# Optimization experiments

Hardware: AMD Instinct MI355X
Metric: run time of the kernel (lower is better)

## Reference

```python
import jax, jax.numpy as jnp
import numpy as np

EPS = 1e-5

def _ln(x, g, b):
    mu = jnp.mean(x, axis=-1, keepdims=True)
    var = jnp.mean(jnp.square(x - mu), axis=-1, keepdims=True)
    return (x - mu) * jax.lax.rsqrt(var + EPS) * g + b

def setup_inputs() -> dict:
    key = jax.random.key(0)
    ks = jax.random.split(key, 12)
    B, N, CZ, CF, CP = 1, 512, 128, 384, 256
    s = 0.02
    return {
        'z': jax.random.normal(ks[0], (B, N, N, CZ), jnp.float32),
        'framepair_embed': jax.random.normal(ks[1], (B, N, N, CP), jnp.float32),
        'rigids_embed_flat': jax.random.normal(ks[2], (B, N, CF), jnp.float32),
        'rigids_to_res_idx': jax.random.randint(ks[3], (B, N), 0, N, dtype=jnp.int64),
        'rigids_mask': jnp.ones((B, N), jnp.float32),
        # nodepair_to_framepair_broadcast: LayerNorm(c_z) + Linear(c_z, c_framepair, bias=False)
        'ln_z_g': jnp.ones((CZ,), jnp.float32),
        'ln_z_b': jnp.zeros((CZ,), jnp.float32),
        'W_z': jax.random.normal(ks[4], (CZ, CP), jnp.float32) * s,
        # frame_ln + two bias-free broadcasts
        'ln_f_g': jnp.ones((CF,), jnp.float32),
        'ln_f_b': jnp.zeros((CF,), jnp.float32),
        'W_l': jax.random.normal(ks[5], (CF, CP), jnp.float32) * s,
        'W_m': jax.random.normal(ks[6], (CF, CP), jnp.float32) * s,
        # framepair_ffn: LN + Linear + ReLU + Linear + ReLU + Linear
        'ffn_ln_g': jnp.ones((CP,), jnp.float32),
        'ffn_ln_b': jnp.zeros((CP,), jnp.float32),
        'W1': jax.random.normal(ks[7], (CP, CP), jnp.float32) * s,
        'b1': jnp.zeros((CP,), jnp.float32),
        'W2': jax.random.normal(ks[8], (CP, CP), jnp.float32) * s,
        'b2': jnp.zeros((CP,), jnp.float32),
        'W3': jax.random.normal(ks[9], (CP, CP), jnp.float32) * s,
        'b3': jnp.zeros((CP,), jnp.float32),
    }

def reference(z, framepair_embed, rigids_embed_flat, rigids_to_res_idx, rigids_mask,
              ln_z_g, ln_z_b, W_z, ln_f_g, ln_f_b, W_l, W_m,
              ffn_ln_g, ffn_ln_b, W1, b1, W2, b2, W3, b3):
    # --- broadcast singles: row + column frame features into pair rep ---
    src = _ln(rigids_embed_flat, ln_f_g, ln_f_b)            # [B, N, CF]
    l = jnp.einsum('bnf,fp->bnp', src, W_l)                 # [B, N, CP]
    m = jnp.einsum('bnf,fp->bnp', src, W_m)
    fe = framepair_embed + l[:, :, None, :] + m[:, None, :, :]
    # --- broadcast pairs: irregular gather of residue-pair features ---
    ii = rigids_to_res_idx[0]                               # [N] (batch-0 indices, as in torch code)
    zb = z[:, ii[:, None], ii[None, :]]                     # [B, N, N, CZ]
    mk = rigids_mask[0]
    pair_mask = (mk[:, None] * mk[None, :])[None, :, :, None]
    zb = zb * pair_mask
    fe = fe + jnp.einsum('bijc,cp->bijp', _ln(zb, ln_z_g, ln_z_b), W_z)
    # --- framepair FFN with residual ---
    h = _ln(fe, ffn_ln_g, ffn_ln_b)
    h = jax.nn.relu(jnp.einsum('bijp,pq->bijq', h, W1) + b1)
    h = jax.nn.relu(jnp.einsum('bijp,pq->bijq', h, W2) + b2)
    fe = fe + jnp.einsum('bijp,pq->bijq', h, W3) + b3
    return fe
```

## Files before the change

kernel.cpp:

```cpp
#include <hip/hip_runtime.h>

#define NN 512
#define CZv 128
#define CFv 384
#define CPv 256
#define ROWS 32

typedef __attribute__((ext_vector_type(8))) short s16x8;
typedef __attribute__((ext_vector_type(4))) short s16x4;
typedef __attribute__((ext_vector_type(4))) float f32x4;

__device__ __forceinline__ unsigned short f2bf(float f) {
  unsigned int u = __builtin_bit_cast(unsigned int, f);
  u = (u + 0x7FFFu + ((u >> 16) & 1u)) >> 16;
  return (unsigned short)u;
}
__device__ __forceinline__ float bf2f(unsigned short h) {
  unsigned int u = ((unsigned int)h) << 16;
  return __builtin_bit_cast(float, u);
}

__global__ void pack_w(const float* __restrict__ W, short* __restrict__ Wf, int total) {
  int o = blockIdx.x * 256 + threadIdx.x;
  if (o >= total) return;
  int e = o & 7;
  int l = (o >> 3) & 63;
  int mt = (o >> 9) & 15;
  int kk = o >> 13;
  int k = kk * 32 + (l >> 4) * 8 + e;
  int p = mt * 16 + (l & 15);
  Wf[o] = (short)f2bf(W[k * 256 + p]);
}

__global__ __launch_bounds__(256) void lm_kernel(
    const float* __restrict__ rf, const float* __restrict__ g, const float* __restrict__ b,
    const float* __restrict__ Wl, const float* __restrict__ Wm,
    float* __restrict__ lout, float* __restrict__ mout) {
  __shared__ float S[8][CFv];
  const int tid = threadIdx.x;
  const int w = tid >> 6;
  const int lane = tid & 63;
  for (int rr = 0; rr < 2; ++rr) {
    int r = blockIdx.x * 8 + w * 2 + rr;
    const float* x = rf + (long)r * CFv;
    float v[6];
    float s1 = 0.f, s2 = 0.f;
#pragma unroll
    for (int q = 0; q < 6; ++q) {
      v[q] = x[lane + q * 64];
      s1 += v[q];
      s2 += v[q] * v[q];
    }
#pragma unroll
    for (int off = 1; off < 64; off <<= 1) {
      s1 += __shfl_xor(s1, off, 64);
      s2 += __shfl_xor(s2, off, 64);
    }
    float mu = s1 * (1.f / CFv);
    float va = s2 * (1.f / CFv) - mu * mu;
    float rs = rsqrtf(va + 1e-5f);
#pragma unroll
    for (int q = 0; q < 6; ++q) {
      int k = lane + q * 64;
      S[w * 2 + rr][k] = (v[q] - mu) * rs * g[k] + b[k];
    }
  }
  __syncthreads();
  float accl[8], accm[8];
#pragma unroll
  for (int r = 0; r < 8; ++r) { accl[r] = 0.f; accm[r] = 0.f; }
  for (int k = 0; k < CFv; ++k) {
    float wl = Wl[k * CPv + tid];
    float wm = Wm[k * CPv + tid];
#pragma unroll
    for (int r = 0; r < 8; ++r) {
      accl[r] += S[r][k] * wl;
      accm[r] += S[r][k] * wm;
    }
  }
#pragma unroll
  for (int r = 0; r < 8; ++r) {
    long rg = blockIdx.x * 8 + r;
    lout[rg * CPv + tid] = accl[r];
    mout[rg * CPv + tid] = accm[r];
  }
}

__global__ __launch_bounds__(256, 3) void fused_main(
    const float* __restrict__ z, const float* __restrict__ fpe,
    const int* __restrict__ idx, const float* __restrict__ msk,
    const float* __restrict__ lnzg, const float* __restrict__ lnzb,
    const float* __restrict__ ffng, const float* __restrict__ ffnb,
    const float* __restrict__ b1p, const float* __restrict__ b2p, const float* __restrict__ b3p,
    const float* __restrict__ lws, const float* __restrict__ mws,
    const short* __restrict__ Wzf, const short* __restrict__ W1f,
    const short* __restrict__ W2f, const short* __restrict__ W3f,
    float* __restrict__ out) {
  __shared__ __align__(16) char X[ROWS * CPv * 2];
  __shared__ __align__(16) char Xres[ROWS * CPv * 2];
  __shared__ float Ssum[4][ROWS];
  __shared__ float Ssq[4][ROWS];

  const int tid = threadIdx.x;
  const int w = tid >> 6;
  const int lane = tid & 63;
  const int l15 = lane & 15;
  const int lg = lane >> 4;

  const int tile = blockIdx.x;
  const int i = tile >> 4;
  const int j0 = (tile & 15) * ROWS;
  const int r0 = tile * ROWS;

  f32x4 fe[2][4];
  {
    f32x4 lb[4];
    const float* lr = lws + (long)i * CPv;
#pragma unroll
    for (int mi = 0; mi < 4; ++mi)
      lb[mi] = *(const f32x4*)(lr + (4 * w + mi) * 16 + lg * 4);
#pragma unroll
    for (int nt = 0; nt < 2; ++nt) {
      const int row = nt * 16 + l15;
      const long rg = (long)r0 + row;
      const float* fpr = fpe + rg * CPv;
      const float* mr = mws + (long)(j0 + row) * CPv;
#pragma unroll
      for (int mi = 0; mi < 4; ++mi) {
        const int c0 = (4 * w + mi) * 16 + lg * 4;
        f32x4 a = *(const f32x4*)(fpr + c0);
        f32x4 mb = *(const f32x4*)(mr + c0);
        fe[nt][mi] = a + lb[mi] + mb;
      }
    }
  }

  {
    const int row = w * 8 + (lane & 7);
    const int seg = (lane >> 3) * 16;
    const int j = j0 + row;
    const int ia = idx[i];
    const int jb = idx[j];
    const float pm = msk[i] * msk[j];
    const float* zr = z + ((long)ia * NN + jb) * CZv + seg;
    f32x4 zv[4];
    float s1 = 0.f, s2 = 0.f;
#pragma unroll
    for (int q = 0; q < 4; ++q) {
      zv[q] = *(const f32x4*)(zr + q * 4);
#pragma unroll
      for (int e = 0; e < 4; ++e) {
        float v = zv[q][e] * pm;
        zv[q][e] = v;
        s1 += v;
        s2 += v * v;
      }
    }
    s1 += __shfl_xor(s1, 8, 64);
    s1 += __shfl_xor(s1, 16, 64);
    s1 += __shfl_xor(s1, 32, 64);
    s2 += __shfl_xor(s2, 8, 64);
    s2 += __shfl_xor(s2, 16, 64);
    s2 += __shfl_xor(s2, 32, 64);
    float mu = s1 * (1.f / CZv);
    float va = s2 * (1.f / CZv) - mu * mu;
    float rs = rsqrtf(va + 1e-5f);
    const int swz = (row & 7) << 4;
#pragma unroll
    for (int h = 0; h < 2; ++h) {
      const f32x4 g0 = *(const f32x4*)(lnzg + seg + h * 8);
      const f32x4 g1 = *(const f32x4*)(lnzg + seg + h * 8 + 4);
      const f32x4 q0 = *(const f32x4*)(lnzb + seg + h * 8);
      const f32x4 q1 = *(const f32x4*)(lnzb + seg + h * 8 + 4);
      s16x8 hv;
#pragma unroll
      for (int e = 0; e < 4; ++e) {
        hv[e] = (short)f2bf((zv[h * 2][e] - mu) * rs * g0[e] + q0[e]);
        hv[4 + e] = (short)f2bf((zv[h * 2 + 1][e] - mu) * rs * g1[e] + q1[e]);
      }
      int off = (row * 256 + seg * 2 + h * 16) ^ swz;
      *(s16x8*)(X + off) = hv;
    }
  }
  __syncthreads();

  {
    const s16x8* Wp = (const s16x8*)Wzf;
    s16x8 af[2][4];
#pragma unroll
    for (int mi = 0; mi < 4; ++mi) af[0][mi] = Wp[(4 * w + mi) * 64 + lane];
    __builtin_amdgcn_s_setprio(1);
#pragma unroll
    for (int kk = 0; kk < 4; ++kk) {
      const int cur = kk & 1;
      if (kk < 3) {
#pragma unroll
        for (int mi = 0; mi < 4; ++mi)
          af[cur ^ 1][mi] = Wp[((kk + 1) * 16 + 4 * w + mi) * 64 + lane];
      }
      s16x8 bfr[2];
#pragma unroll
      for (int nt = 0; nt < 2; ++nt) {
        const int row = nt * 16 + l15;
        int off = (row * 256 + kk * 64 + lg * 16) ^ ((row & 7) << 4);
        bfr[nt] = *(const s16x8*)(X + off);
      }
#pragma unroll
      for (int mi = 0; mi < 4; ++mi)
#pragma unroll
        for (int nt = 0; nt < 2; ++nt)
          fe[nt][mi] = __builtin_amdgcn_mfma_f32_16x16x32_bf16(af[cur][mi], bfr[nt], fe[nt][mi], 0, 0, 0);
    }
    __builtin_amdgcn_s_setprio(0);
  }

  float mu2[2], rs2[2];
  {
    float s[2], q[2];
#pragma unroll
    for (int nt = 0; nt < 2; ++nt) {
      s[nt] = 0.f;
      q[nt] = 0.f;
#pragma unroll
      for (int mi = 0; mi < 4; ++mi)
#pragma unroll
        for (int e = 0; e < 4; ++e) {
          float v = fe[nt][mi][e];
          s[nt] += v;
          q[nt] += v * v;
        }
      s[nt] += __shfl_xor(s[nt], 16, 64);
      s[nt] += __shfl_xor(s[nt], 32, 64);
      q[nt] += __shfl_xor(q[nt], 16, 64);
      q[nt] += __shfl_xor(q[nt], 32, 64);
    }
    if (lane < 16) {
#pragma unroll
      for (int nt = 0; nt < 2; ++nt) {
        Ssum[w][nt * 16 + lane] = s[nt];
        Ssq[w][nt * 16 + lane] = q[nt];
      }
    }
    __syncthreads();
#pragma unroll
    for (int nt = 0; nt < 2; ++nt) {
      const int row = nt * 16 + l15;
      float ts = Ssum[0][row] + Ssum[1][row] + Ssum[2][row] + Ssum[3][row];
      float tq = Ssq[0][row] + Ssq[1][row] + Ssq[2][row] + Ssq[3][row];
      float mu = ts * (1.f / CPv);
      float va = tq * (1.f / CPv) - mu * mu;
      mu2[nt] = mu;
      rs2[nt] = rsqrtf(va + 1e-5f);
    }
  }

#pragma unroll
  for (int mi = 0; mi < 4; ++mi) {
    const int c0 = (4 * w + mi) * 16 + lg * 4;
    const f32x4 g4 = *(const f32x4*)(ffng + c0);
    const f32x4 b4 = *(const f32x4*)(ffnb + c0);
#pragma unroll
    for (int nt = 0; nt < 2; ++nt) {
      const int row = nt * 16 + l15;
      const int swz = (row & 7) << 4;
      s16x4 hv, fv;
#pragma unroll
      for (int e = 0; e < 4; ++e) {
        float v = fe[nt][mi][e];
        hv[e] = (short)f2bf((v - mu2[nt]) * rs2[nt] * g4[e] + b4[e]);
        fv[e] = (short)f2bf(v);
      }
      int off = (row * 512 + c0 * 2) ^ swz;
      *(s16x4*)(X + off) = hv;
      *(s16x4*)(Xres + off) = fv;
    }
  }
  __syncthreads();

  auto ffn_gemm = [&](const short* Wf, f32x4(&acc)[2][4]) {
    const s16x8* Wp = (const s16x8*)Wf;
    s16x8 af[2][4];
#pragma unroll
    for (int mi = 0; mi < 4; ++mi) af[0][mi] = Wp[(4 * w + mi) * 64 + lane];
    __builtin_amdgcn_s_setprio(1);
#pragma unroll
    for (int kk = 0; kk < 8; ++kk) {
      const int cur = kk & 1;
      if (kk < 7) {
#pragma unroll
        for (int mi = 0; mi < 4; ++mi)
          af[cur ^ 1][mi] = Wp[((kk + 1) * 16 + 4 * w + mi) * 64 + lane];
      }
      s16x8 bfr[2];
#pragma unroll
      for (int nt = 0; nt < 2; ++nt) {
        const int row = nt * 16 + l15;
        int off = (row * 512 + kk * 64 + lg * 16) ^ ((row & 7) << 4);
        bfr[nt] = *(const s16x8*)(X + off);
      }
#pragma unroll
      for (int mi = 0; mi < 4; ++mi)
#pragma unroll
        for (int nt = 0; nt < 2; ++nt)
          acc[nt][mi] = __builtin_amdgcn_mfma_f32_16x16x32_bf16(af[cur][mi], bfr[nt], acc[nt][mi], 0, 0, 0);
    }
    __builtin_amdgcn_s_setprio(0);
  };

  auto write_relu = [&](f32x4(&acc)[2][4]) {
#pragma unroll
    for (int nt = 0; nt < 2; ++nt) {
      const int row = nt * 16 + l15;
      const int swz = (row & 7) << 4;
#pragma unroll
      for (int mi = 0; mi < 4; ++mi) {
        const int c0 = (4 * w + mi) * 16 + lg * 4;
        s16x4 hv;
#pragma unroll
        for (int e = 0; e < 4; ++e) {
          float v = acc[nt][mi][e];
          v = v > 0.f ? v : 0.f;
          hv[e] = (short)f2bf(v);
        }
        int off = (row * 512 + c0 * 2) ^ swz;
        *(s16x4*)(X + off) = hv;
      }
    }
  };

  f32x4 hacc[2][4];
#pragma unroll
  for (int mi = 0; mi < 4; ++mi) {
    const f32x4 bini = *(const f32x4*)(b1p + (4 * w + mi) * 16 + lg * 4);
#pragma unroll
    for (int nt = 0; nt < 2; ++nt) hacc[nt][mi] = bini;
  }
  ffn_gemm(W1f, hacc);
  __syncthreads();
  write_relu(hacc);
  __syncthreads();

#pragma unroll
  for (int mi = 0; mi < 4; ++mi) {
    const f32x4 bini = *(const f32x4*)(b2p + (4 * w + mi) * 16 + lg * 4);
#pragma unroll
    for (int nt = 0; nt < 2; ++nt) hacc[nt][mi] = bini;
  }
  ffn_gemm(W2f, hacc);
  __syncthreads();
  write_relu(hacc);
  __syncthreads();

#pragma unroll
  for (int mi = 0; mi < 4; ++mi) {
    const f32x4 b34 = *(const f32x4*)(b3p + (4 * w + mi) * 16 + lg * 4);
    const int c0 = (4 * w + mi) * 16 + lg * 4;
#pragma unroll
    for (int nt = 0; nt < 2; ++nt) {
      const int row = nt * 16 + l15;
      const int swz = (row & 7) << 4;
      int off = (row * 512 + c0 * 2) ^ swz;
      s16x4 fv = *(const s16x4*)(Xres + off);
#pragma unroll
      for (int e = 0; e < 4; ++e)
        hacc[nt][mi][e] = bf2f((unsigned short)fv[e]) + b34[e];
    }
  }
  ffn_gemm(W3f, hacc);
#pragma unroll
  for (int nt = 0; nt < 2; ++nt) {
    const long rg = (long)r0 + nt * 16 + l15;
#pragma unroll
    for (int mi = 0; mi < 4; ++mi) {
      const int c0 = (4 * w + mi) * 16 + lg * 4;
      *(f32x4*)(out + rg * CPv + c0) = hacc[nt][mi];
    }
  }
}

extern "C" void kernel_launch(void* const* d_in, const int* in_sizes, int n_in,
                              void* d_out, int out_size, void* d_ws, size_t ws_size,
                              hipStream_t stream) {
  const float* z = (const float*)d_in[0];
  const float* fpe = (const float*)d_in[1];
  const float* rf = (const float*)d_in[2];
  const int* idx = (const int*)d_in[3];
  const float* msk = (const float*)d_in[4];
  const float* lnzg = (const float*)d_in[5];
  const float* lnzb = (const float*)d_in[6];
  const float* Wz = (const float*)d_in[7];
  const float* lnfg = (const float*)d_in[8];
  const float* lnfb = (const float*)d_in[9];
  const float* Wl = (const float*)d_in[10];
  const float* Wm = (const float*)d_in[11];
  const float* ffng = (const float*)d_in[12];
  const float* ffnb = (const float*)d_in[13];
  const float* W1 = (const float*)d_in[14];
  const float* b1 = (const float*)d_in[15];
  const float* W2 = (const float*)d_in[16];
  const float* b2 = (const float*)d_in[17];
  const float* W3 = (const float*)d_in[18];
  const float* b3 = (const float*)d_in[19];
  float* out = (float*)d_out;

  char* ws = (char*)d_ws;
  float* lws = (float*)ws;
  float* mws = (float*)(ws + 512 * 1024);
  short* Wzf = (short*)(ws + 1024 * 1024);
  short* W1f = (short*)(ws + 1024 * 1024 + 64 * 1024);
  short* W2f = (short*)(ws + 1024 * 1024 + 192 * 1024);
  short* W3f = (short*)(ws + 1024 * 1024 + 320 * 1024);

  pack_w<<<128, 256, 0, stream>>>(Wz, Wzf, 128 * 256);
  pack_w<<<256, 256, 0, stream>>>(W1, W1f, 256 * 256);
  pack_w<<<256, 256, 0, stream>>>(W2, W2f, 256 * 256);
  pack_w<<<256, 256, 0, stream>>>(W3, W3f, 256 * 256);
  lm_kernel<<<64, 256, 0, stream>>>(rf, lnfg, lnfb, Wl, Wm, lws, mws);
  fused_main<<<8192, 256, 0, stream>>>(z, fpe, idx, msk, lnzg, lnzb, ffng, ffnb,
                                       b1, b2, b3, lws, mws, Wzf, W1f, W2f, W3f, out);
}
```

Before: 350.6 us.

## Remap tiles across XCDs, rotate K order per tile, alias LN scratch into X

Block indices are remapped so consecutive blocks on the same XCD process contiguous tiles, which improves L2 locality for the z/fpe/m rows. Each tile rotates its K-chunk order by tile index (XOR), so concurrent blocks fetch different weight slices and global/L2 hotspots on the weight arrays are spread out. The FFN GEMM loop is rewritten as a non-unrolled two-stage ping-pong with explicit register double buffering, which shrinks code size and register pressure. The LN reduction scratch is aliased into the X shared buffer, cutting LDS use at the cost of an extra barrier.

```diff
diff --git a/kernel.cpp b/kernel.cpp
--- a/kernel.cpp
+++ b/kernel.cpp
@@ -98,8 +98,8 @@
     float* __restrict__ out) {
   __shared__ __align__(16) char X[ROWS * CPv * 2];
   __shared__ __align__(16) char Xres[ROWS * CPv * 2];
-  __shared__ float Ssum[4][ROWS];
-  __shared__ float Ssq[4][ROWS];
+  float* SS = (float*)(X + 8192);
+  float* SQ = (float*)(X + 8192 + 512);
 
   const int tid = threadIdx.x;
   const int w = tid >> 6;
@@ -107,10 +107,13 @@
   const int l15 = lane & 15;
   const int lg = lane >> 4;
 
-  const int tile = blockIdx.x;
+  const int b = blockIdx.x;
+  const int tile = (b & 7) * 1024 + (b >> 3);
   const int i = tile >> 4;
   const int j0 = (tile & 15) * ROWS;
   const int r0 = tile * ROWS;
+  const int rotz = tile & 3;
+  const int rotf = tile & 7;
 
   f32x4 fe[2][4];
   {
@@ -186,30 +189,65 @@
 
   {
     const s16x8* Wp = (const s16x8*)Wzf;
-    s16x8 af[2][4];
-#pragma unroll
-    for (int mi = 0; mi < 4; ++mi) af[0][mi] = Wp[(4 * w + mi) * 64 + lane];
+    const int base = 4 * w;
+    const int cswz = (lg * 16) ^ ((l15 & 7) << 4);
+    s16x8 af0[4], af1[4];
+#pragma unroll
+    for (int mi = 0; mi < 4; ++mi) af0[mi] = Wp[((0 ^ rotz) * 16 + base + mi) * 64 + lane];
+#pragma unroll
+    for (int mi = 0; mi < 4; ++mi) af1[mi] = Wp[((1 ^ rotz) * 16 + base + mi) * 64 + lane];
     __builtin_amdgcn_s_setprio(1);
-#pragma unroll
-    for (int kk = 0; kk < 4; ++kk) {
-      const int cur = kk & 1;
-      if (kk < 3) {
-#pragma unroll
-        for (int mi = 0; mi < 4; ++mi)
-          af[cur ^ 1][mi] = Wp[((kk + 1) * 16 + 4 * w + mi) * 64 + lane];
-      }
+    {
+      const int krc = 0 ^ rotz;
       s16x8 bfr[2];
 #pragma unroll
-      for (int nt = 0; nt < 2; ++nt) {
-        const int row = nt * 16 + l15;
-        int off = (row * 256 + kk * 64 + lg * 16) ^ ((row & 7) << 4);
-        bfr[nt] = *(const s16x8*)(X + off);
-      }
+      for (int nt = 0; nt < 2; ++nt)
+        bfr[nt] = *(const s16x8*)(X + (nt * 16 + l15) * 256 + ((krc * 64) ^ cswz));
 #pragma unroll
       for (int mi = 0; mi < 4; ++mi)
 #pragma unroll
         for (int nt = 0; nt < 2; ++nt)
-          fe[nt][mi] = __builtin_amdgcn_mfma_f32_16x16x32_bf16(af[cur][mi], bfr[nt], fe[nt][mi], 0, 0, 0);
+          fe[nt][mi] = __builtin_amdgcn_mfma_f32_16x16x32_bf16(af0[mi], bfr[nt], fe[nt][mi], 0, 0, 0);
+    }
+#pragma unroll
+    for (int mi = 0; mi < 4; ++mi) af0[mi] = Wp[((2 ^ rotz) * 16 + base + mi) * 64 + lane];
+    {
+      const int krc = 1 ^ rotz;
+      s16x8 bfr[2];
+#pragma unroll
+      for (int nt = 0; nt < 2; ++nt)
+        bfr[nt] = *(const s16x8*)(X + (nt * 16 + l15) * 256 + ((krc * 64) ^ cswz));
+#pragma unroll
+      for (int mi = 0; mi < 4; ++mi)
+#pragma unroll
+        for (int nt = 0; nt < 2; ++nt)
+          fe[nt][mi] = __builtin_amdgcn_mfma_f32_16x16x32_bf16(af1[mi], bfr[nt], fe[nt][mi], 0, 0, 0);
+    }
+#pragma unroll
+    for (int mi = 0; mi < 4; ++mi) af1[mi] = Wp[((3 ^ rotz) * 16 + base + mi) * 64 + lane];
+    {
+      const int krc = 2 ^ rotz;
+      s16x8 bfr[2];
+#pragma unroll
+      for (int nt = 0; nt < 2; ++nt)
+        bfr[nt] = *(const s16x8*)(X + (nt * 16 + l15) * 256 + ((krc * 64) ^ cswz));
+#pragma unroll
+      for (int mi = 0; mi < 4; ++mi)
+#pragma unroll
+        for (int nt = 0; nt < 2; ++nt)
+          fe[nt][mi] = __builtin_amdgcn_mfma_f32_16x16x32_bf16(af0[mi], bfr[nt], fe[nt][mi], 0, 0, 0);
+    }
+    {
+      const int krc = 3 ^ rotz;
+      s16x8 bfr[2];
+#pragma unroll
+      for (int nt = 0; nt < 2; ++nt)
+        bfr[nt] = *(const s16x8*)(X + (nt * 16 + l15) * 256 + ((krc * 64) ^ cswz));
+#pragma unroll
+      for (int mi = 0; mi < 4; ++mi)
+#pragma unroll
+        for (int nt = 0; nt < 2; ++nt)
+          fe[nt][mi] = __builtin_amdgcn_mfma_f32_16x16x32_bf16(af1[mi], bfr[nt], fe[nt][mi], 0, 0, 0);
     }
     __builtin_amdgcn_s_setprio(0);
   }
@@ -237,22 +275,23 @@
     if (lane < 16) {
 #pragma unroll
       for (int nt = 0; nt < 2; ++nt) {
-        Ssum[w][nt * 16 + lane] = s[nt];
-        Ssq[w][nt * 16 + lane] = q[nt];
+        SS[w * 32 + nt * 16 + lane] = s[nt];
+        SQ[w * 32 + nt * 16 + lane] = q[nt];
       }
     }
     __syncthreads();
 #pragma unroll
     for (int nt = 0; nt < 2; ++nt) {
       const int row = nt * 16 + l15;
-      float ts = Ssum[0][row] + Ssum[1][row] + Ssum[2][row] + Ssum[3][row];
-      float tq = Ssq[0][row] + Ssq[1][row] + Ssq[2][row] + Ssq[3][row];
+      float ts = SS[row] + SS[32 + row] + SS[64 + row] + SS[96 + row];
+      float tq = SQ[row] + SQ[32 + row] + SQ[64 + row] + SQ[96 + row];
       float mu = ts * (1.f / CPv);
       float va = tq * (1.f / CPv) - mu * mu;
       mu2[nt] = mu;
       rs2[nt] = rsqrtf(va + 1e-5f);
     }
   }
+  __syncthreads();
 
 #pragma unroll
   for (int mi = 0; mi < 4; ++mi) {
@@ -279,30 +318,48 @@
 
   auto ffn_gemm = [&](const short* Wf, f32x4(&acc)[2][4]) {
     const s16x8* Wp = (const s16x8*)Wf;
-    s16x8 af[2][4];
-#pragma unroll
-    for (int mi = 0; mi < 4; ++mi) af[0][mi] = Wp[(4 * w + mi) * 64 + lane];
+    const int base = 4 * w;
+    const int cswz = (lg * 16) ^ ((l15 & 7) << 4);
+    s16x8 af0[4], af1[4];
+#pragma unroll
+    for (int mi = 0; mi < 4; ++mi) af0[mi] = Wp[((0 ^ rotf) * 16 + base + mi) * 64 + lane];
     __builtin_amdgcn_s_setprio(1);
-#pragma unroll
-    for (int kk = 0; kk < 8; ++kk) {
-      const int cur = kk & 1;
-      if (kk < 7) {
+#pragma unroll 1
+    for (int kk = 0; kk < 8; kk += 2) {
+      {
+        const int kr = (kk + 1) ^ rotf;
+#pragma unroll
+        for (int mi = 0; mi < 4; ++mi) af1[mi] = Wp[(kr * 16 + base + mi) * 64 + lane];
+      }
+      {
+        const int krc = kk ^ rotf;
+        s16x8 bfr[2];
+#pragma unroll
+        for (int nt = 0; nt < 2; ++nt)
+          bfr[nt] = *(const s16x8*)(X + (nt * 16 + l15) * 512 + ((krc * 64) ^ cswz));
 #pragma unroll
         for (int mi = 0; mi < 4; ++mi)
-          af[cur ^ 1][mi] = Wp[((kk + 1) * 16 + 4 * w + mi) * 64 + lane];
-      }
-      s16x8 bfr[2];
-#pragma unroll
-      for (int nt = 0; nt < 2; ++nt) {
-        const int row = nt * 16 + l15;
-        int off = (row * 512 + kk * 64 + lg * 16) ^ ((row & 7) << 4);
-        bfr[nt] = *(const s16x8*)(X + off);
-      }
-#pragma unroll
-      for (int mi = 0; mi < 4; ++mi)
-#pragma unroll
-        for (int nt = 0; nt < 2; ++nt)
-          acc[nt][mi] = __builtin_amdgcn_mfma_f32_16x16x32_bf16(af[cur][mi], bfr[nt], acc[nt][mi], 0, 0, 0);
+#pragma unroll
+          for (int nt = 0; nt < 2; ++nt)
+            acc[nt][mi] = __builtin_amdgcn_mfma_f32_16x16x32_bf16(af0[mi], bfr[nt], acc[nt][mi], 0, 0, 0);
+      }
+      if (kk + 2 < 8) {
+        const int kr = (kk + 2) ^ rotf;
+#pragma unroll
+        for (int mi = 0; mi < 4; ++mi) af0[mi] = Wp[(kr * 16 + base + mi) * 64 + lane];
+      }
+      {
+        const int krc = (kk + 1) ^ rotf;
+        s16x8 bfr[2];
+#pragma unroll
+        for (int nt = 0; nt < 2; ++nt)
+          bfr[nt] = *(const s16x8*)(X + (nt * 16 + l15) * 512 + ((krc * 64) ^ cswz));
+#pragma unroll
+        for (int mi = 0; mi < 4; ++mi)
+#pragma unroll
+          for (int nt = 0; nt < 2; ++nt)
+            acc[nt][mi] = __builtin_amdgcn_mfma_f32_16x16x32_bf16(af1[mi], bfr[nt], acc[nt][mi], 0, 0, 0);
+      }
     }
     __builtin_amdgcn_s_setprio(0);
   };
```

Result: slower. 365.7 us (+4.3%).

## Ping-pong LDS buffers, keep residual in registers, swizzle tile order, raise occupancy

Applied to the files above, without the earlier changes.

The residual copy of the framepair features now stays in registers as packed bf16 instead of LDS. This frees the second LDS buffer, which becomes a ping-pong buffer for the FFN hidden activations, so one barrier between each GEMM and its ReLU write-back can be dropped. The block-to-tile mapping is permuted with a stride of 8, and launch bounds request 4 waves per SIMD instead of 3. The aims are less barrier stall and higher occupancy, at the cost of more register pressure, which may cause spills under the tighter bound.

```diff
diff --git a/kernel.cpp b/kernel.cpp
--- a/kernel.cpp
+++ b/kernel.cpp
@@ -86,7 +86,7 @@
   }
 }
 
-__global__ __launch_bounds__(256, 3) void fused_main(
+__global__ __launch_bounds__(256, 4) void fused_main(
     const float* __restrict__ z, const float* __restrict__ fpe,
     const int* __restrict__ idx, const float* __restrict__ msk,
     const float* __restrict__ lnzg, const float* __restrict__ lnzb,
@@ -97,7 +97,7 @@
     const short* __restrict__ W2f, const short* __restrict__ W3f,
     float* __restrict__ out) {
   __shared__ __align__(16) char X[ROWS * CPv * 2];
-  __shared__ __align__(16) char Xres[ROWS * CPv * 2];
+  __shared__ __align__(16) char X2[ROWS * CPv * 2];
   __shared__ float Ssum[4][ROWS];
   __shared__ float Ssq[4][ROWS];
 
@@ -107,7 +107,8 @@
   const int l15 = lane & 15;
   const int lg = lane >> 4;
 
-  const int tile = blockIdx.x;
+  const int b = blockIdx.x;
+  const int tile = (b & 7) * 1024 + (b >> 3);
   const int i = tile >> 4;
   const int j0 = (tile & 15) * ROWS;
   const int r0 = tile * ROWS;
@@ -254,6 +255,7 @@
     }
   }
 
+  s16x4 fe16[2][4];
 #pragma unroll
   for (int mi = 0; mi < 4; ++mi) {
     const int c0 = (4 * w + mi) * 16 + lg * 4;
@@ -270,14 +272,14 @@
         hv[e] = (short)f2bf((v - mu2[nt]) * rs2[nt] * g4[e] + b4[e]);
         fv[e] = (short)f2bf(v);
       }
+      fe16[nt][mi] = fv;
       int off = (row * 512 + c0 * 2) ^ swz;
       *(s16x4*)(X + off) = hv;
-      *(s16x4*)(Xres + off) = fv;
     }
   }
   __syncthreads();
 
-  auto ffn_gemm = [&](const short* Wf, f32x4(&acc)[2][4]) {
+  auto ffn_gemm = [&](const short* Wf, const char* Xb, f32x4(&acc)[2][4]) {
     const s16x8* Wp = (const s16x8*)Wf;
     s16x8 af[2][4];
 #pragma unroll
@@ -296,7 +298,7 @@
       for (int nt = 0; nt < 2; ++nt) {
         const int row = nt * 16 + l15;
         int off = (row * 512 + kk * 64 + lg * 16) ^ ((row & 7) << 4);
-        bfr[nt] = *(const s16x8*)(X + off);
+        bfr[nt] = *(const s16x8*)(Xb + off);
       }
 #pragma unroll
       for (int mi = 0; mi < 4; ++mi)
@@ -307,7 +309,7 @@
     __builtin_amdgcn_s_setprio(0);
   };
 
-  auto write_relu = [&](f32x4(&acc)[2][4]) {
+  auto write_relu = [&](char* Xb, f32x4(&acc)[2][4]) {
 #pragma unroll
     for (int nt = 0; nt < 2; ++nt) {
       const int row = nt * 16 + l15;
@@ -323,7 +325,7 @@
           hv[e] = (short)f2bf(v);
         }
         int off = (row * 512 + c0 * 2) ^ swz;
-        *(s16x4*)(X + off) = hv;
+        *(s16x4*)(Xb + off) = hv;
       }
     }
   };
@@ -335,9 +337,8 @@
 #pragma unroll
     for (int nt = 0; nt < 2; ++nt) hacc[nt][mi] = bini;
   }
-  ffn_gemm(W1f, hacc);
-  __syncthreads();
-  write_relu(hacc);
+  ffn_gemm(W1f, X, hacc);
+  write_relu(X2, hacc);
   __syncthreads();
 
 #pragma unroll
@@ -346,27 +347,20 @@
 #pragma unroll
     for (int nt = 0; nt < 2; ++nt) hacc[nt][mi] = bini;
   }
-  ffn_gemm(W2f, hacc);
-  __syncthreads();
-  write_relu(hacc);
+  ffn_gemm(W2f, X2, hacc);
+  write_relu(X, hacc);
   __syncthreads();
 
 #pragma unroll
   for (int mi = 0; mi < 4; ++mi) {
     const f32x4 b34 = *(const f32x4*)(b3p + (4 * w + mi) * 16 + lg * 4);
-    const int c0 = (4 * w + mi) * 16 + lg * 4;
-#pragma unroll
-    for (int nt = 0; nt < 2; ++nt) {
-      const int row = nt * 16 + l15;
-      const int swz = (row & 7) << 4;
-      int off = (row * 512 + c0 * 2) ^ swz;
-      s16x4 fv = *(const s16x4*)(Xres + off);
+#pragma unroll
+    for (int nt = 0; nt < 2; ++nt)
 #pragma unroll
       for (int e = 0; e < 4; ++e)
-        hacc[nt][mi][e] = bf2f((unsigned short)fv[e]) + b34[e];
-    }
-  }
-  ffn_gemm(W3f, hacc);
+        hacc[nt][mi][e] = bf2f((unsigned short)fe16[nt][mi][e]) + b34[e];
+  }
+  ffn_gemm(W3f, X, hacc);
 #pragma unroll
   for (int nt = 0; nt < 2; ++nt) {
     const long rg = (long)r0 + nt * 16 + l15;
```

Measured after the change: 451.7 us. +28.8%, slower.
